# Performance work log

Hardware: AMD Instinct MI355X
Metric: run time of the kernel (lower is better)

The kernel has to match this reference:

```python
import jax, jax.numpy as jnp
import numpy as np

B, S, D, H, L, F = 4, 2048, 512, 8, 4, 2048
DH = D // H
EPS = 1e-5


def setup_inputs() -> dict:
    key = jax.random.key(0)
    ks = jax.random.split(key, 16)
    sc = 0.02
    inp = {
        "turn_embeddings": jax.random.normal(ks[0], (B, S, D), jnp.float32),
        "Wqkv": jax.random.normal(ks[1], (L, 3 * D, D), jnp.float32) * sc,
        "bqkv": jnp.zeros((L, 3 * D), jnp.float32),
        "Wo": jax.random.normal(ks[2], (L, D, D), jnp.float32) * sc,
        "bo": jnp.zeros((L, D), jnp.float32),
        "W1": jax.random.normal(ks[3], (L, F, D), jnp.float32) * sc,
        "b1": jnp.zeros((L, F), jnp.float32),
        "W2": jax.random.normal(ks[4], (L, D, F), jnp.float32) * sc,
        "b2": jnp.zeros((L, D), jnp.float32),
        "ln1_g": jnp.ones((L, D), jnp.float32),
        "ln1_b": jnp.zeros((L, D), jnp.float32),
        "ln2_g": jnp.ones((L, D), jnp.float32),
        "ln2_b": jnp.zeros((L, D), jnp.float32),
        "speaker_ids": jax.random.randint(ks[5], (B, S), 0, 4, jnp.int64 if jax.config.jax_enable_x64 else jnp.int32),
    }
    return inp


def _layer_norm(x, g, b):
    mu = jnp.mean(x, axis=-1, keepdims=True)
    var = jnp.mean(jnp.square(x - mu), axis=-1, keepdims=True)
    return (x - mu) * jax.lax.rsqrt(var + EPS) * g + b


def _attention(x, Wqkv, bqkv, Wo, bo, allow):
    # x: [B,S,D]; allow: [B,1,S,S] boolean (causal & same-speaker)
    qkv = x @ Wqkv.T + bqkv                       # [B,S,3D]
    q, k, v = jnp.split(qkv, 3, axis=-1)
    q = q.reshape(x.shape[0], x.shape[1], H, DH)
    k = k.reshape(x.shape[0], x.shape[1], H, DH)
    v = v.reshape(x.shape[0], x.shape[1], H, DH)
    scores = jnp.einsum("bqhd,bkhd->bhqk", q, k) / np.sqrt(DH)
    scores = jnp.where(allow, scores, jnp.finfo(scores.dtype).min)
    p = jax.nn.softmax(scores, axis=-1)
    o = jnp.einsum("bhqk,bkhd->bqhd", p, v).reshape(x.shape[0], x.shape[1], D)
    return o @ Wo.T + bo


def reference(turn_embeddings, Wqkv, bqkv, Wo, bo, W1, b1, W2, b2,
              ln1_g, ln1_b, ln2_g, ln2_b, speaker_ids):
    Bc, Sc, _ = turn_embeddings.shape
    causal = jnp.tril(jnp.ones((Sc, Sc), bool))                 # [S,S]
    same = speaker_ids[:, :, None] == speaker_ids[:, None, :]    # [B,S,S]
    allow = (same & causal)[:, None, :, :]                       # [B,1,S,S]
    x = turn_embeddings
    for l in range(L):
        a = _attention(x, Wqkv[l], bqkv[l], Wo[l], bo[l], allow)
        x = _layer_norm(x + a, ln1_g[l], ln1_b[l])
        h = jax.nn.relu(x @ W1[l].T + b1[l]) @ W2[l].T + b2[l]
        x = _layer_norm(x + h, ln2_g[l], ln2_b[l])
    return x
```

## Files before the change

kernel.cpp:

```cpp
#include <hip/hip_runtime.h>
#include <stdint.h>

#define BN 4
#define SN 2048
#define DN 512
#define HN 8
#define LN 4
#define FN 2048
#define MN (BN * SN)
#define TD (3 * DN)

typedef __attribute__((ext_vector_type(8))) __bf16 bf16x8;
typedef __attribute__((ext_vector_type(4))) float f32x4;
typedef __attribute__((ext_vector_type(8))) unsigned short ushortx8;

static __device__ __forceinline__ unsigned short f2bf(float f) {
    return __builtin_bit_cast(unsigned short, (__bf16)f);
}
static __device__ __forceinline__ float bf2f(unsigned short h) {
    return __builtin_bit_cast(float, (uint32_t)h << 16);
}

static __device__ __forceinline__ void gload16(const void* g, void* l) {
    __builtin_amdgcn_global_load_lds(
        (const __attribute__((address_space(1))) void*)g,
        (__attribute__((address_space(3))) void*)l, 16, 0, 0);
}

__global__ __launch_bounds__(256) void k_cvt_all(const float* __restrict__ Wqkv,
                                                 const float* __restrict__ Wo,
                                                 const float* __restrict__ W1,
                                                 const float* __restrict__ W2,
                                                 const float* __restrict__ te,
                                                 unsigned short* __restrict__ wqkv_b,
                                                 unsigned short* __restrict__ wo_b,
                                                 unsigned short* __restrict__ w1_b,
                                                 unsigned short* __restrict__ w2_b,
                                                 unsigned short* __restrict__ xb) {
    constexpr int G0 = LN * TD * DN / 4;
    constexpr int G1 = G0 + LN * DN * DN / 4;
    constexpr int G2 = G1 + LN * FN * DN / 4;
    constexpr int G3 = G2 + LN * DN * FN / 4;
    constexpr int G4 = G3 + MN * DN / 4;
    int i = blockIdx.x * blockDim.x + threadIdx.x;
    int stride = gridDim.x * blockDim.x;
    for (; i < G4; i += stride) {
        const float* s; unsigned short* d; int j;
        if (i < G0)      { s = Wqkv; d = wqkv_b; j = i; }
        else if (i < G1) { s = Wo;   d = wo_b;   j = i - G0; }
        else if (i < G2) { s = W1;   d = w1_b;   j = i - G1; }
        else if (i < G3) { s = W2;   d = w2_b;   j = i - G2; }
        else             { s = te;   d = xb;     j = i - G3; }
        float4 v = ((const float4*)s)[j];
        ushort4 o;
        o.x = f2bf(v.x); o.y = f2bf(v.y); o.z = f2bf(v.z); o.w = f2bf(v.w);
        ((ushort4*)d)[j] = o;
    }
}

template <int MODE, int BNT>
__global__ __launch_bounds__(256) void k_gemm(const unsigned short* __restrict__ A,
                                              const unsigned short* __restrict__ B,
                                              const float* __restrict__ bias,
                                              unsigned short* __restrict__ Cb,
                                              int M, int N, int K, int GX) {
    __shared__ __align__(16) unsigned short As[128][64];
    __shared__ __align__(16) unsigned short Bs[BNT][64];
    constexpr int NFR = BNT / 32;

    const int t = threadIdx.x;
    const int lane = t & 63;
    const int wid = t >> 6;
    const int wm = wid >> 1, wn = wid & 1;
    const int lr = lane & 15;
    const int lg = lane >> 4;

    const int nwg = gridDim.x;
    const int bid = blockIdx.x;
    const int swz = (bid & 7) * (nwg >> 3) + (bid >> 3);
    const int bx = swz % GX;
    const int by = swz / GX;

    const size_t rowA = (size_t)by * 128;
    const size_t rowB = (size_t)bx * BNT;
    const unsigned short* Ab = A + rowA * K;
    const unsigned short* Bb = B + rowB * K;

    const int srow = lane >> 3;
    const int sgran = (lane & 7) ^ srow;

    f32x4 acc[4][NFR] = {};

    for (int k0 = 0; k0 < K; k0 += 64) {
        __syncthreads();
#pragma unroll
        for (int j = 0; j < 4; ++j) {
            const int c = wid * 4 + j;
            const size_t goff = (size_t)(8 * c + srow) * K + k0 + sgran * 8;
            gload16(Ab + goff, &As[8 * c][0]);
        }
#pragma unroll
        for (int j = 0; j < NFR; ++j) {
            const int c = wid * NFR + j;
            const size_t goff = (size_t)(8 * c + srow) * K + k0 + sgran * 8;
            gload16(Bb + goff, &Bs[8 * c][0]);
        }
        __syncthreads();

#pragma unroll
        for (int h = 0; h < 2; ++h) {
            const int gp = (h * 4 + lg) ^ (lr & 7);
            bf16x8 af[4], bfr[NFR];
#pragma unroll
            for (int mi = 0; mi < 4; ++mi)
                af[mi] = *(const bf16x8*)&As[wm * 64 + mi * 16 + lr][gp * 8];
#pragma unroll
            for (int ni = 0; ni < NFR; ++ni)
                bfr[ni] = *(const bf16x8*)&Bs[wn * (BNT / 2) + ni * 16 + lr][gp * 8];
#pragma unroll
            for (int mi = 0; mi < 4; ++mi)
#pragma unroll
                for (int ni = 0; ni < NFR; ++ni)
                    acc[mi][ni] = __builtin_amdgcn_mfma_f32_16x16x32_bf16(
                        af[mi], bfr[ni], acc[mi][ni], 0, 0, 0);
        }
    }

    float bv[NFR];
#pragma unroll
    for (int ni = 0; ni < NFR; ++ni)
        bv[ni] = bias[(int)rowB + wn * (BNT / 2) + ni * 16 + lr];

#pragma unroll
    for (int mi = 0; mi < 4; ++mi) {
#pragma unroll
        for (int ni = 0; ni < NFR; ++ni) {
            int col = (int)rowB + wn * (BNT / 2) + ni * 16 + lr;
            int row0 = (int)rowA + wm * 64 + mi * 16 + lg * 4;
#pragma unroll
            for (int r = 0; r < 4; ++r) {
                float v = acc[mi][ni][r] + bv[ni];
                if (MODE == 2) v = fmaxf(v, 0.f);
                Cb[(size_t)(row0 + r) * N + col] = f2bf(v);
            }
        }
    }
}

__global__ __launch_bounds__(256) void k_attn(const unsigned short* __restrict__ qkv,
                                              const int* __restrict__ spk,
                                              unsigned short* __restrict__ o) {
    __shared__ __align__(16) unsigned short Ks[2][64][64];
    __shared__ __align__(16) unsigned short Vt[2][64][64];
    __shared__ __align__(16) unsigned short Ps[4][16][64];

    const int t = threadIdx.x;
    const int lane = t & 63;
    const int w = t >> 6;
    const int lr = lane & 15;
    const int lg = lane >> 4;
    const int l7 = lr & 7;

    const int wg = blockIdx.x;
    const int inner = wg >> 3;
    const int bh = 4 * (wg & 7) + (inner & 3);
    const int qtile = (SN / 64 - 1) - (inner >> 2);
    const int b = bh >> 3;
    const int h = bh & 7;
    const int qb = qtile * 64;

    const size_t base = (size_t)b * SN * TD;
    const unsigned short* kg = qkv + base + DN + h * 64;
    const unsigned short* vg = qkv + base + 2 * DN + h * 64;

    const float SCL = 0.125f * 1.4426950408889634f;
    const unsigned short* qptr = qkv + base + (size_t)(qb + w * 16 + lr) * TD + h * 64;
    bf16x8 aq0 = *(const bf16x8*)(qptr + lg * 8);
    bf16x8 aq1 = *(const bf16x8*)(qptr + 32 + lg * 8);
#pragma unroll
    for (int j = 0; j < 8; ++j) {
        aq0[j] = (__bf16)((float)aq0[j] * SCL);
        aq1[j] = (__bf16)((float)aq1[j] * SCL);
    }

    int sqr[4], qrow[4];
#pragma unroll
    for (int r = 0; r < 4; ++r) {
        qrow[r] = qb + w * 16 + lg * 4 + r;
        sqr[r] = spk[b * SN + qrow[r]];
    }

    const int krl = lane >> 3;
    const int kgran = (lane & 7) ^ krl;
    const int vrow = lane;
    const int vd0 = w * 16;

#pragma unroll
    for (int j = 0; j < 2; ++j)
        gload16(kg + (size_t)(w * 16 + j * 8 + krl) * TD + kgran * 8,
                &Ks[0][w * 16 + j * 8][0]);
    ushortx8 vra = *(const ushortx8*)&vg[(size_t)vrow * TD + vd0];
    ushortx8 vrb = *(const ushortx8*)&vg[(size_t)vrow * TD + vd0 + 8];
#pragma unroll
    for (int j = 0; j < 8; ++j) {
        const int vc0 = (((vrow >> 3) ^ j) << 3) + (vrow & 7);
        Vt[0][vd0 + j][vc0] = vra[j];
        Vt[0][vd0 + 8 + j][vc0] = vrb[j];
    }

    float lsum[4] = {0.f, 0.f, 0.f, 0.f};
    f32x4 acc_o[4] = {};

    const int ntiles = qtile + 1;
    for (int it = 0; it < ntiles; ++it) {
        const int k0 = it * 64;
        const int cur = it & 1;
        __syncthreads();

        const bool nx = (it + 1 < ntiles);
        if (nx) {
            const int kn = k0 + 64;
#pragma unroll
            for (int j = 0; j < 2; ++j)
                gload16(kg + (size_t)(kn + w * 16 + j * 8 + krl) * TD + kgran * 8,
                        &Ks[cur ^ 1][w * 16 + j * 8][0]);
            vra = *(const ushortx8*)&vg[(size_t)(kn + vrow) * TD + vd0];
            vrb = *(const ushortx8*)&vg[(size_t)(kn + vrow) * TD + vd0 + 8];
        }
        int skr[4];
#pragma unroll
        for (int ni = 0; ni < 4; ++ni) skr[ni] = spk[b * SN + k0 + 16 * ni + lr];

        f32x4 sc4[4] = {};
        __builtin_amdgcn_s_setprio(1);
#pragma unroll
        for (int ni = 0; ni < 4; ++ni) {
            bf16x8 bk0 = *(const bf16x8*)&Ks[cur][16 * ni + lr][(lg ^ l7) * 8];
            bf16x8 bk1 = *(const bf16x8*)&Ks[cur][16 * ni + lr][((lg + 4) ^ l7) * 8];
            sc4[ni] = __builtin_amdgcn_mfma_f32_16x16x32_bf16(aq0, bk0, sc4[ni], 0, 0, 0);
            sc4[ni] = __builtin_amdgcn_mfma_f32_16x16x32_bf16(aq1, bk1, sc4[ni], 0, 0, 0);
        }
        __builtin_amdgcn_s_setprio(0);

        const bool diag = (it == ntiles - 1);
#pragma unroll
        for (int ni = 0; ni < 4; ++ni) {
#pragma unroll
            for (int r = 0; r < 4; ++r) {
                bool allow = (skr[ni] == sqr[r]);
                if (diag) allow = allow && (16 * ni + lr <= w * 16 + lg * 4 + r);
                float p = allow ? __builtin_amdgcn_exp2f(sc4[ni][r]) : 0.f;
                lsum[r] += p;
                const int q7 = (lg * 4 + r) & 7;
                const int pg = ((2 * ni + (lr >> 3)) ^ q7) * 8 + l7;
                Ps[w][lg * 4 + r][pg] = f2bf(p);
            }
        }

        bf16x8 ap0 = *(const bf16x8*)&Ps[w][lr][(lg ^ l7) * 8];
        bf16x8 ap1 = *(const bf16x8*)&Ps[w][lr][((lg + 4) ^ l7) * 8];
        __builtin_amdgcn_s_setprio(1);
#pragma unroll
        for (int ni = 0; ni < 4; ++ni) {
            bf16x8 bv0 = *(const bf16x8*)&Vt[cur][16 * ni + lr][(lg ^ l7) * 8];
            bf16x8 bv1 = *(const bf16x8*)&Vt[cur][16 * ni + lr][((lg + 4) ^ l7) * 8];
            acc_o[ni] = __builtin_amdgcn_mfma_f32_16x16x32_bf16(ap0, bv0, acc_o[ni], 0, 0, 0);
            acc_o[ni] = __builtin_amdgcn_mfma_f32_16x16x32_bf16(ap1, bv1, acc_o[ni], 0, 0, 0);
        }
        __builtin_amdgcn_s_setprio(0);

        if (nx) {
            const int nb = cur ^ 1;
#pragma unroll
            for (int j = 0; j < 8; ++j) {
                const int vc0 = (((vrow >> 3) ^ j) << 3) + (vrow & 7);
                Vt[nb][vd0 + j][vc0] = vra[j];
                Vt[nb][vd0 + 8 + j][vc0] = vrb[j];
            }
        }
    }

#pragma unroll
    for (int r = 0; r < 4; ++r) {
        float s = lsum[r];
        s += __shfl_xor(s, 1);
        s += __shfl_xor(s, 2);
        s += __shfl_xor(s, 4);
        s += __shfl_xor(s, 8);
        float inv = 1.f / s;
#pragma unroll
        for (int ni = 0; ni < 4; ++ni) {
            int d = 16 * ni + lr;
            o[(size_t)(b * SN + qrow[r]) * DN + h * 64 + d] = f2bf(acc_o[ni][r] * inv);
        }
    }
}

template <bool XF32>
__global__ __launch_bounds__(256) void k_add_ln(const void* __restrict__ xin_,
                                                const unsigned short* __restrict__ dl,
                                                const float* __restrict__ g,
                                                const float* __restrict__ bta,
                                                unsigned short* __restrict__ xb,
                                                float* __restrict__ fout) {
    const int row = blockIdx.x * 4 + (threadIdx.x >> 6);
    const int lane = threadIdx.x & 63;
    const size_t off = (size_t)row * DN + lane * 8;
    const int c0 = lane * 8;

    float v[8];
    if (XF32) {
        const float* xin = (const float*)xin_;
        float4 a0 = *(const float4*)&xin[off];
        float4 a1 = *(const float4*)&xin[off + 4];
        v[0] = a0.x; v[1] = a0.y; v[2] = a0.z; v[3] = a0.w;
        v[4] = a1.x; v[5] = a1.y; v[6] = a1.z; v[7] = a1.w;
    } else {
        ushortx8 xa = *(const ushortx8*)&((const unsigned short*)xin_)[off];
#pragma unroll
        for (int i = 0; i < 8; ++i) v[i] = bf2f(xa[i]);
    }
    ushortx8 dd = *(const ushortx8*)&dl[off];
#pragma unroll
    for (int i = 0; i < 8; ++i) v[i] += bf2f(dd[i]);

    float s1 = 0.f, s2 = 0.f;
#pragma unroll
    for (int i = 0; i < 8; ++i) { s1 += v[i]; s2 += v[i] * v[i]; }
#pragma unroll
    for (int msk = 32; msk; msk >>= 1) {
        s1 += __shfl_xor(s1, msk);
        s2 += __shfl_xor(s2, msk);
    }
    const float mean = s1 * (1.f / 512.f);
    const float var = s2 * (1.f / 512.f) - mean * mean;
    const float rs = rsqrtf(var + 1e-5f);

    float4 g0 = *(const float4*)&g[c0];
    float4 g1 = *(const float4*)&g[c0 + 4];
    float4 b0 = *(const float4*)&bta[c0];
    float4 b1 = *(const float4*)&bta[c0 + 4];
    float gg[8] = {g0.x, g0.y, g0.z, g0.w, g1.x, g1.y, g1.z, g1.w};
    float bb[8] = {b0.x, b0.y, b0.z, b0.w, b1.x, b1.y, b1.z, b1.w};

    float y[8];
    ushortx8 ub;
#pragma unroll
    for (int i = 0; i < 8; ++i) {
        y[i] = (v[i] - mean) * rs * gg[i] + bb[i];
        ub[i] = f2bf(y[i]);
    }
    *(ushortx8*)&xb[off] = ub;
    if (fout) {
        *(float4*)&fout[off] = make_float4(y[0], y[1], y[2], y[3]);
        *(float4*)&fout[off + 4] = make_float4(y[4], y[5], y[6], y[7]);
    }
}

extern "C" void kernel_launch(void* const* d_in, const int* in_sizes, int n_in,
                              void* d_out, int out_size, void* d_ws, size_t ws_size,
                              hipStream_t stream) {
    const float* te   = (const float*)d_in[0];
    const float* Wqkv = (const float*)d_in[1];
    const float* bqkv = (const float*)d_in[2];
    const float* Wo   = (const float*)d_in[3];
    const float* bo   = (const float*)d_in[4];
    const float* W1   = (const float*)d_in[5];
    const float* b1   = (const float*)d_in[6];
    const float* W2   = (const float*)d_in[7];
    const float* b2   = (const float*)d_in[8];
    const float* g1   = (const float*)d_in[9];
    const float* be1  = (const float*)d_in[10];
    const float* g2   = (const float*)d_in[11];
    const float* be2  = (const float*)d_in[12];
    const int*   spk  = (const int*)d_in[13];
    float* out = (float*)d_out;

    char* ws = (char*)d_ws;
    size_t off = 0;
    auto alloc = [&](size_t bytes) -> char* {
        char* p = ws + off;
        off += (bytes + 255) & ~(size_t)255;
        return p;
    };
    unsigned short* wqkv_b = (unsigned short*)alloc((size_t)LN * TD * DN * 2);
    unsigned short* wo_b   = (unsigned short*)alloc((size_t)LN * DN * DN * 2);
    unsigned short* w1_b   = (unsigned short*)alloc((size_t)LN * FN * DN * 2);
    unsigned short* w2_b   = (unsigned short*)alloc((size_t)LN * DN * FN * 2);
    unsigned short* xb     = (unsigned short*)alloc((size_t)MN * DN * 2);
    unsigned short* u      = (unsigned short*)alloc((size_t)MN * FN * 2);
    unsigned short* ob     = (unsigned short*)alloc((size_t)MN * DN * 2);
    unsigned short* projb  = (unsigned short*)alloc((size_t)MN * DN * 2);
    unsigned short* qkvb = u;
    unsigned short* hb   = u;

    k_cvt_all<<<2048, 256, 0, stream>>>(Wqkv, Wo, W1, W2, te,
                                        wqkv_b, wo_b, w1_b, w2_b, xb);

    for (int l = 0; l < LN; ++l) {
        k_gemm<1, 128><<<(MN / 128) * (TD / 128), 256, 0, stream>>>(
            xb, wqkv_b + (size_t)l * TD * DN, bqkv + l * TD, qkvb,
            MN, TD, DN, TD / 128);
        k_attn<<<(SN / 64) * BN * HN, 256, 0, stream>>>(qkvb, spk, ob);
        k_gemm<1, 64><<<(MN / 128) * (DN / 64), 256, 0, stream>>>(
            ob, wo_b + (size_t)l * DN * DN, bo + l * DN, projb,
            MN, DN, DN, DN / 64);
        if (l == 0)
            k_add_ln<true><<<MN / 4, 256, 0, stream>>>(
                te, projb, g1 + l * DN, be1 + l * DN, xb, nullptr);
        else
            k_add_ln<false><<<MN / 4, 256, 0, stream>>>(
                xb, projb, g1 + l * DN, be1 + l * DN, xb, nullptr);
        k_gemm<2, 128><<<(MN / 128) * (FN / 128), 256, 0, stream>>>(
            xb, w1_b + (size_t)l * FN * DN, b1 + l * FN, hb,
            MN, FN, DN, FN / 128);
        k_gemm<1, 64><<<(MN / 128) * (DN / 64), 256, 0, stream>>>(
            hb, w2_b + (size_t)l * DN * FN, b2 + l * DN, projb,
            MN, DN, FN, DN / 64);
        k_add_ln<false><<<MN / 4, 256, 0, stream>>>(
            xb, projb, g2 + l * DN, be2 + l * DN, xb,
            (l == LN - 1) ? out : nullptr);
    }
    (void)in_sizes; (void)n_in; (void)out_size; (void)ws_size;
}
```

Measured before the change: 606.6 us.

## Shrink N=512 GEMM tiles to 64x64, register-stage K tiles, skip last bf16 store

The GEMM kernel gains a templated M-tile size, and the Wo and W2 projections (N=512) now use 64x64 tiles. This doubles the grid to 1024 blocks, giving more blocks per CU at the cost of less operand reuse per block. Attention K tiles are now loaded through registers and written to LDS with a swizzled layout, matching the V path, instead of using direct global-to-LDS loads. The final layer norm no longer writes the unused bf16 copy when it writes the fp32 output.

```diff
diff --git a/kernel.cpp b/kernel.cpp
--- a/kernel.cpp
+++ b/kernel.cpp
@@ -58,14 +58,15 @@
     }
 }
 
-template <int MODE, int BNT>
+template <int MODE, int BMT, int BNT>
 __global__ __launch_bounds__(256) void k_gemm(const unsigned short* __restrict__ A,
                                               const unsigned short* __restrict__ B,
                                               const float* __restrict__ bias,
                                               unsigned short* __restrict__ Cb,
                                               int M, int N, int K, int GX) {
-    __shared__ __align__(16) unsigned short As[128][64];
+    __shared__ __align__(16) unsigned short As[BMT][64];
     __shared__ __align__(16) unsigned short Bs[BNT][64];
+    constexpr int MFR = BMT / 32;
     constexpr int NFR = BNT / 32;
 
     const int t = threadIdx.x;
@@ -81,7 +82,7 @@
     const int bx = swz % GX;
     const int by = swz / GX;
 
-    const size_t rowA = (size_t)by * 128;
+    const size_t rowA = (size_t)by * BMT;
     const size_t rowB = (size_t)bx * BNT;
     const unsigned short* Ab = A + rowA * K;
     const unsigned short* Bb = B + rowB * K;
@@ -89,13 +90,13 @@
     const int srow = lane >> 3;
     const int sgran = (lane & 7) ^ srow;
 
-    f32x4 acc[4][NFR] = {};
+    f32x4 acc[MFR][NFR] = {};
 
     for (int k0 = 0; k0 < K; k0 += 64) {
         __syncthreads();
 #pragma unroll
-        for (int j = 0; j < 4; ++j) {
-            const int c = wid * 4 + j;
+        for (int j = 0; j < MFR; ++j) {
+            const int c = wid * MFR + j;
             const size_t goff = (size_t)(8 * c + srow) * K + k0 + sgran * 8;
             gload16(Ab + goff, &As[8 * c][0]);
         }
@@ -110,15 +111,15 @@
 #pragma unroll
         for (int h = 0; h < 2; ++h) {
             const int gp = (h * 4 + lg) ^ (lr & 7);
-            bf16x8 af[4], bfr[NFR];
-#pragma unroll
-            for (int mi = 0; mi < 4; ++mi)
-                af[mi] = *(const bf16x8*)&As[wm * 64 + mi * 16 + lr][gp * 8];
+            bf16x8 af[MFR], bfr[NFR];
+#pragma unroll
+            for (int mi = 0; mi < MFR; ++mi)
+                af[mi] = *(const bf16x8*)&As[wm * (BMT / 2) + mi * 16 + lr][gp * 8];
 #pragma unroll
             for (int ni = 0; ni < NFR; ++ni)
                 bfr[ni] = *(const bf16x8*)&Bs[wn * (BNT / 2) + ni * 16 + lr][gp * 8];
 #pragma unroll
-            for (int mi = 0; mi < 4; ++mi)
+            for (int mi = 0; mi < MFR; ++mi)
 #pragma unroll
                 for (int ni = 0; ni < NFR; ++ni)
                     acc[mi][ni] = __builtin_amdgcn_mfma_f32_16x16x32_bf16(
@@ -132,11 +133,11 @@
         bv[ni] = bias[(int)rowB + wn * (BNT / 2) + ni * 16 + lr];
 
 #pragma unroll
-    for (int mi = 0; mi < 4; ++mi) {
+    for (int mi = 0; mi < MFR; ++mi) {
 #pragma unroll
         for (int ni = 0; ni < NFR; ++ni) {
             int col = (int)rowB + wn * (BNT / 2) + ni * 16 + lr;
-            int row0 = (int)rowA + wm * 64 + mi * 16 + lg * 4;
+            int row0 = (int)rowA + wm * (BMT / 2) + mi * 16 + lg * 4;
 #pragma unroll
             for (int r = 0; r < 4; ++r) {
                 float v = acc[mi][ni][r] + bv[ni];
@@ -190,17 +191,17 @@
         sqr[r] = spk[b * SN + qrow[r]];
     }
 
-    const int krl = lane >> 3;
-    const int kgran = (lane & 7) ^ krl;
-    const int vrow = lane;
-    const int vd0 = w * 16;
-
-#pragma unroll
-    for (int j = 0; j < 2; ++j)
-        gload16(kg + (size_t)(w * 16 + j * 8 + krl) * TD + kgran * 8,
-                &Ks[0][w * 16 + j * 8][0]);
+    const int kr0 = t >> 3;
+    const int kgr = ((t & 7) ^ (kr0 & 7)) * 8;
+    const int vrow = t & 63;
+    const int vd0 = (t >> 6) * 16;
+
+    uint4 kra = *(const uint4*)&kg[(size_t)kr0 * TD + (t & 7) * 8];
+    uint4 krb = *(const uint4*)&kg[(size_t)(kr0 + 32) * TD + (t & 7) * 8];
     ushortx8 vra = *(const ushortx8*)&vg[(size_t)vrow * TD + vd0];
     ushortx8 vrb = *(const ushortx8*)&vg[(size_t)vrow * TD + vd0 + 8];
+    *(uint4*)&Ks[0][kr0][kgr] = kra;
+    *(uint4*)&Ks[0][kr0 + 32][kgr] = krb;
 #pragma unroll
     for (int j = 0; j < 8; ++j) {
         const int vc0 = (((vrow >> 3) ^ j) << 3) + (vrow & 7);
@@ -220,10 +221,8 @@
         const bool nx = (it + 1 < ntiles);
         if (nx) {
             const int kn = k0 + 64;
-#pragma unroll
-            for (int j = 0; j < 2; ++j)
-                gload16(kg + (size_t)(kn + w * 16 + j * 8 + krl) * TD + kgran * 8,
-                        &Ks[cur ^ 1][w * 16 + j * 8][0]);
+            kra = *(const uint4*)&kg[(size_t)(kn + kr0) * TD + (t & 7) * 8];
+            krb = *(const uint4*)&kg[(size_t)(kn + kr0 + 32) * TD + (t & 7) * 8];
             vra = *(const ushortx8*)&vg[(size_t)(kn + vrow) * TD + vd0];
             vrb = *(const ushortx8*)&vg[(size_t)(kn + vrow) * TD + vd0 + 8];
         }
@@ -271,6 +270,8 @@
 
         if (nx) {
             const int nb = cur ^ 1;
+            *(uint4*)&Ks[nb][kr0][kgr] = kra;
+            *(uint4*)&Ks[nb][kr0 + 32][kgr] = krb;
 #pragma unroll
             for (int j = 0; j < 8; ++j) {
                 const int vc0 = (((vrow >> 3) ^ j) << 3) + (vrow & 7);
@@ -344,16 +345,18 @@
     float bb[8] = {b0.x, b0.y, b0.z, b0.w, b1.x, b1.y, b1.z, b1.w};
 
     float y[8];
-    ushortx8 ub;
-#pragma unroll
-    for (int i = 0; i < 8; ++i) {
+#pragma unroll
+    for (int i = 0; i < 8; ++i)
         y[i] = (v[i] - mean) * rs * gg[i] + bb[i];
-        ub[i] = f2bf(y[i]);
-    }
-    *(ushortx8*)&xb[off] = ub;
+
     if (fout) {
         *(float4*)&fout[off] = make_float4(y[0], y[1], y[2], y[3]);
         *(float4*)&fout[off + 4] = make_float4(y[4], y[5], y[6], y[7]);
+    } else {
+        ushortx8 ub;
+#pragma unroll
+        for (int i = 0; i < 8; ++i) ub[i] = f2bf(y[i]);
+        *(ushortx8*)&xb[off] = ub;
     }
 }
 
@@ -398,11 +401,11 @@
                                         wqkv_b, wo_b, w1_b, w2_b, xb);
 
     for (int l = 0; l < LN; ++l) {
-        k_gemm<1, 128><<<(MN / 128) * (TD / 128), 256, 0, stream>>>(
+        k_gemm<1, 128, 128><<<(MN / 128) * (TD / 128), 256, 0, stream>>>(
             xb, wqkv_b + (size_t)l * TD * DN, bqkv + l * TD, qkvb,
             MN, TD, DN, TD / 128);
         k_attn<<<(SN / 64) * BN * HN, 256, 0, stream>>>(qkvb, spk, ob);
-        k_gemm<1, 64><<<(MN / 128) * (DN / 64), 256, 0, stream>>>(
+        k_gemm<1, 64, 64><<<(MN / 64) * (DN / 64), 256, 0, stream>>>(
             ob, wo_b + (size_t)l * DN * DN, bo + l * DN, projb,
             MN, DN, DN, DN / 64);
         if (l == 0)
@@ -411,10 +414,10 @@
         else
             k_add_ln<false><<<MN / 4, 256, 0, stream>>>(
                 xb, projb, g1 + l * DN, be1 + l * DN, xb, nullptr);
-        k_gemm<2, 128><<<(MN / 128) * (FN / 128), 256, 0, stream>>>(
+        k_gemm<2, 128, 128><<<(MN / 128) * (FN / 128), 256, 0, stream>>>(
             xb, w1_b + (size_t)l * FN * DN, b1 + l * FN, hb,
             MN, FN, DN, FN / 128);
-        k_gemm<1, 64><<<(MN / 128) * (DN / 64), 256, 0, stream>>>(
+        k_gemm<1, 64, 64><<<(MN / 64) * (DN / 64), 256, 0, stream>>>(
             hb, w2_b + (size_t)l * DN * FN, b2 + l * DN, projb,
             MN, DN, FN, DN / 64);
         k_add_ln<false><<<MN / 4, 256, 0, stream>>>(
```

Result: faster. 579.9 us, median of 2 (-4.4%).
